# Performance work log

Measured on AMD Instinct MI355X. Metric: run time of the kernel, lower is better.

## Reference

```python
import jax, jax.numpy as jnp
import numpy as np

ALPHA = 0.2  # LeakyReLU negative slope (init arg `alpha`)
N, F_IN, F_OUT = 8192, 512, 256


def setup_inputs() -> dict:
    key = jax.random.key(0)
    k1, k2, k3, k4 = jax.random.split(key, 4)
    x = jax.random.normal(k1, (N, F_IN), dtype=jnp.float32)
    adj = jax.random.randint(k2, (N, N), 0, 2, dtype=jnp.int32)
    W = jax.random.normal(k3, (F_IN, F_OUT), dtype=jnp.float32) * (1.0 / np.sqrt(F_IN))
    a = jax.random.normal(k4, (2 * F_OUT, 1), dtype=jnp.float32) * (1.0 / np.sqrt(F_IN))
    return {"x": x, "adj": adj, "W": W, "a": a}


def reference(x, adj, W, a):
    h = x @ W  # [N, F_OUT]
    f_out = W.shape[1]
    # e[i,j] = LeakyReLU(a1 . h_i + a2 . h_j); computed without the O(N^2*2F) concat
    f1 = h @ a[:f_out, 0]   # [N]
    f2 = h @ a[f_out:, 0]   # [N]
    s = f1[:, None] + f2[None, :]  # [N, N]
    e = jnp.where(s >= 0, s, ALPHA * s)
    # Faithful to the source bug: -9e15 * zeros_like == zeros, so masked entries are 0.0
    att = jnp.where(adj > 0, e, jnp.zeros((), dtype=e.dtype))
    att = jax.nn.softmax(att, axis=1)
    # dropout is identity in eval mode
    h_prime = att @ h  # [N, F_OUT]
    return jax.nn.elu(h_prime)  # concat=True branch
```

## Files before the change

### kernel.cpp

```cpp
#include <hip/hip_runtime.h>
#include <stdint.h>

#define NN 8192
#define FIN 512
#define FOUT 256
#define ALPHA 0.2f
#define KSPLIT 8
#define KSLICE (NN / KSPLIT)
#define BK 32
#define ITERS (KSLICE / BK)

typedef float f32x4 __attribute__((ext_vector_type(4)));
typedef short s16x8 __attribute__((ext_vector_type(8)));

__device__ __forceinline__ uint16_t f2bf(float f) {
  union { float f; uint32_t u; } v; v.f = f;
  uint32_t u = v.u + 0x7fffu + ((v.u >> 16) & 1u);
  return (uint16_t)(u >> 16);
}

__device__ __forceinline__ void lds_barrier() {
  asm volatile("s_waitcnt lgkmcnt(0)\n\ts_barrier" ::: "memory");
}

__global__ __launch_bounds__(256) void k_wa(const float* __restrict__ W,
                                            const float* __restrict__ a,
                                            float* __restrict__ wa1, float* __restrict__ wa2) {
  __shared__ float a1[256], a2[256];
  int tid = threadIdx.x;
  a1[tid] = a[tid];
  a2[tid] = a[tid + 256];
  __syncthreads();
  int m = blockIdx.x * 256 + tid;
  const float* wrow = W + (size_t)m * FOUT;
  float s1 = 0.f, s2 = 0.f;
  for (int k = 0; k < FOUT; k += 4) {
    f32x4 v = *(const f32x4*)(wrow + k);
#pragma unroll
    for (int i = 0; i < 4; i++) {
      s1 += v[i] * a1[k + i];
      s2 += v[i] * a2[k + i];
    }
  }
  wa1[m] = s1; wa2[m] = s2;
}

__global__ __launch_bounds__(256) void k_f1f2(const float* __restrict__ x,
                                              const float* __restrict__ wa1,
                                              const float* __restrict__ wa2,
                                              float* __restrict__ f1, float* __restrict__ f2) {
  __shared__ float s1[512], s2[512];
  int tid = threadIdx.x;
  s1[tid] = wa1[tid]; s1[tid + 256] = wa1[tid + 256];
  s2[tid] = wa2[tid]; s2[tid + 256] = wa2[tid + 256];
  __syncthreads();
  int w = tid >> 6, l = tid & 63;
  int row = blockIdx.x * 4 + w;
  const float* xr = x + (size_t)row * FIN + l * 8;
  f32x4 v0 = *(const f32x4*)xr;
  f32x4 v1 = *(const f32x4*)(xr + 4);
  int kb = l * 8;
  float d1 = 0.f, d2 = 0.f;
#pragma unroll
  for (int i = 0; i < 4; i++) {
    d1 += v0[i] * s1[kb + i] + v1[i] * s1[kb + 4 + i];
    d2 += v0[i] * s2[kb + i] + v1[i] * s2[kb + 4 + i];
  }
#pragma unroll
  for (int off = 32; off; off >>= 1) {
    d1 += __shfl_down(d1, off);
    d2 += __shfl_down(d2, off);
  }
  if (l == 0) { f1[row] = d1; f2[row] = d2; }
}

__global__ __launch_bounds__(256) void k_prep_wt(const float* __restrict__ W,
                                                 uint16_t* __restrict__ wt) {
  int idx = blockIdx.x * 256 + threadIdx.x;
  int f  = idx >> 7;
  int k4 = (idx & 127) * 4;
  ushort4 o;
  o.x = f2bf(W[(size_t)(k4 + 0) * FOUT + f]);
  o.y = f2bf(W[(size_t)(k4 + 1) * FOUT + f]);
  o.z = f2bf(W[(size_t)(k4 + 2) * FOUT + f]);
  o.w = f2bf(W[(size_t)(k4 + 3) * FOUT + f]);
  *(ushort4*)(wt + (size_t)f * FIN + k4) = o;
}

__global__ __launch_bounds__(256, 2) void k_gemm_h(const float* __restrict__ x,
                                                   const uint16_t* __restrict__ wt,
                                                   uint16_t* __restrict__ ht) {
  __shared__ __align__(16) uint16_t Xs[64][40];
  __shared__ __align__(16) uint16_t Ws[128][40];
  int i0 = blockIdx.x * 64;
  int f0 = blockIdx.y * 128;
  int tid = threadIdx.x;
  int l = tid & 63, w = tid >> 6;
  int q = l >> 4, r16 = l & 15;
  f32x4 acc[4][2];
#pragma unroll
  for (int a = 0; a < 4; a++)
#pragma unroll
    for (int b = 0; b < 2; b++) acc[a][b] = (f32x4)0.f;

  int xr = tid >> 2, xc = (tid & 3) * 8;
  int wr = tid >> 1, wc = (tid & 1) * 16;
  const float* xp = x + (size_t)(i0 + xr) * FIN + xc;
  const uint16_t* wp = wt + (size_t)(f0 + wr) * FIN + wc;

  f32x4 u0 = *(const f32x4*)xp;
  f32x4 u1 = *(const f32x4*)(xp + 4);
  uint4 wA = *(const uint4*)wp;
  uint4 wB = *(const uint4*)(wp + 8);

  const int GI = FIN / BK;
  for (int s = 0; s < GI; s++) {
    int sn = (s + 1 < GI) ? (s + 1) : s;
    f32x4 u0n = *(const f32x4*)(xp + sn * BK);
    f32x4 u1n = *(const f32x4*)(xp + sn * BK + 4);
    uint4 wAn = *(const uint4*)(wp + sn * BK);
    uint4 wBn = *(const uint4*)(wp + sn * BK + 8);

    uint4 pk;
    pk.x = (uint32_t)f2bf(u0[0]) | ((uint32_t)f2bf(u0[1]) << 16);
    pk.y = (uint32_t)f2bf(u0[2]) | ((uint32_t)f2bf(u0[3]) << 16);
    pk.z = (uint32_t)f2bf(u1[0]) | ((uint32_t)f2bf(u1[1]) << 16);
    pk.w = (uint32_t)f2bf(u1[2]) | ((uint32_t)f2bf(u1[3]) << 16);
    *(uint4*)(&Xs[xr][xc]) = pk;
    *(uint4*)(&Ws[wr][wc]) = wA;
    *(uint4*)(&Ws[wr][wc + 8]) = wB;
    lds_barrier();

    s16x8 Af[4], Bf[2];
#pragma unroll
    for (int a = 0; a < 4; a++) Af[a] = *(const s16x8*)(&Xs[a * 16 + r16][q * 8]);
#pragma unroll
    for (int b = 0; b < 2; b++) Bf[b] = *(const s16x8*)(&Ws[w * 32 + b * 16 + r16][q * 8]);
#pragma unroll
    for (int a = 0; a < 4; a++)
#pragma unroll
      for (int b = 0; b < 2; b++)
        acc[a][b] = __builtin_amdgcn_mfma_f32_16x16x32_bf16(Af[a], Bf[b], acc[a][b], 0, 0, 0);
    lds_barrier();
    u0 = u0n; u1 = u1n; wA = wAn; wB = wBn;
  }

#pragma unroll
  for (int a = 0; a < 4; a++)
#pragma unroll
    for (int b = 0; b < 2; b++) {
      int f = f0 + w * 32 + b * 16 + r16;
      int i = i0 + a * 16 + q * 4;
      ushort4 o;
      o.x = f2bf(acc[a][b][0]); o.y = f2bf(acc[a][b][1]);
      o.z = f2bf(acc[a][b][2]); o.w = f2bf(acc[a][b][3]);
      *(ushort4*)(ht + (size_t)f * NN + i) = o;
    }
}

__global__ __launch_bounds__(256) void k_zero(float* __restrict__ l_arr) {
  l_arr[blockIdx.x * 256 + threadIdx.x] = 0.f;
}

__global__ __launch_bounds__(256, 3) void k_att(const int* __restrict__ adj,
                                                const uint16_t* __restrict__ ht,
                                                const float* __restrict__ f1,
                                                const float* __restrict__ f2,
                                                float* __restrict__ l_arr,
                                                float* __restrict__ part) {
  __shared__ __align__(16) uint16_t Ps[2][64][40];
  __shared__ __align__(16) float Fs[KSLICE];
  const int i0 = blockIdx.x * 64;
  const int jbase = blockIdx.y * KSLICE;
  const int tid = threadIdx.x;
  const int l = tid & 63, w = tid >> 6;
  const int q = l >> 4, r16 = l & 15;
  const int pr = tid >> 2, pc = tid & 3;

  *(f32x4*)(&Fs[tid * 4]) = *(const f32x4*)(f2 + jbase + tid * 4);

  const float f1i = f1[i0 + pr];
  float lsum = 0.f;
  f32x4 acc[4][4];
#pragma unroll
  for (int a = 0; a < 4; a++)
#pragma unroll
    for (int b = 0; b < 4; b++) acc[a][b] = (f32x4)0.f;

  const int* adjp = adj + (size_t)(i0 + pr) * NN + jbase + pc * 8;
  const uint16_t* htb = ht + (size_t)(w * 64 + r16) * NN + jbase + q * 8;

  int4 adjR0[2], adjR1[2];
  s16x8 Bf0[4], Bf1[4];

#define LOADADJ(t, R) do {                                    \
    int t_ = ((t) < ITERS) ? (t) : (ITERS - 1);               \
    const int* ap_ = adjp + t_ * BK;                          \
    R[0] = *(const int4*)ap_;                                 \
    R[1] = *(const int4*)(ap_ + 4);                           \
  } while (0)

#define LOADB(t, B) do {                                      \
    int t_ = ((t) < ITERS) ? (t) : (ITERS - 1);               \
    const uint16_t* hp_ = htb + t_ * BK;                      \
    B[0] = *(const s16x8*)(hp_);                              \
    B[1] = *(const s16x8*)(hp_ + (size_t)16 * NN);            \
    B[2] = *(const s16x8*)(hp_ + (size_t)32 * NN);            \
    B[3] = *(const s16x8*)(hp_ + (size_t)48 * NN);            \
  } while (0)

#define STAGE(t, R, buf) do {                                 \
    f32x4 F0_ = *(const f32x4*)(&Fs[(t) * BK + pc * 8]);      \
    f32x4 F1_ = *(const f32x4*)(&Fs[(t) * BK + pc * 8 + 4]);  \
    const int* av_ = (const int*)&R[0];                       \
    s16x8 pv_;                                                \
    _Pragma("unroll")                                         \
    for (int i_ = 0; i_ < 8; i_++) {                          \
      float fj_ = (i_ < 4) ? F0_[i_] : F1_[i_ - 4];           \
      float s_ = f1i + fj_;                                   \
      float e_ = fmaxf(s_, ALPHA * s_);                       \
      float p2_ = (av_[i_] != 0) ? __expf(e_) : 1.0f;         \
      lsum += p2_;                                            \
      pv_[i_] = (short)f2bf(p2_);                             \
    }                                                         \
    *(s16x8*)(&Ps[buf][pr][pc * 8]) = pv_;                    \
  } while (0)

#define MFMA_(B, buf) do {                                    \
    s16x8 Af_[4];                                             \
    _Pragma("unroll")                                         \
    for (int a_ = 0; a_ < 4; a_++)                            \
      Af_[a_] = *(const s16x8*)(&Ps[buf][a_ * 16 + r16][q * 8]); \
    _Pragma("unroll")                                         \
    for (int a_ = 0; a_ < 4; a_++)                            \
      _Pragma("unroll")                                       \
      for (int b_ = 0; b_ < 4; b_++)                          \
        acc[a_][b_] = __builtin_amdgcn_mfma_f32_16x16x32_bf16(Af_[a_], B[b_], acc[a_][b_], 0, 0, 0); \
  } while (0)

  LOADADJ(0, adjR0); LOADADJ(1, adjR1);
  LOADB(0, Bf0);     LOADB(1, Bf1);
  lds_barrier();
  STAGE(0, adjR0, 0);
  LOADADJ(2, adjR0);
  lds_barrier();

  for (int s = 0; s < ITERS - 2; s += 2) {
    MFMA_(Bf0, 0);
    LOADB(s + 2, Bf0);
    STAGE(s + 1, adjR1, 1);
    LOADADJ(s + 3, adjR1);
    lds_barrier();

    MFMA_(Bf1, 1);
    LOADB(s + 3, Bf1);
    STAGE(s + 2, adjR0, 0);
    LOADADJ(s + 4, adjR0);
    lds_barrier();
  }
  MFMA_(Bf0, 0);
  STAGE(ITERS - 1, adjR1, 1);
  lds_barrier();
  MFMA_(Bf1, 1);

#undef LOADADJ
#undef LOADB
#undef STAGE
#undef MFMA_

  lsum += __shfl_down(lsum, 2);
  lsum += __shfl_down(lsum, 1);
  if (pc == 0) atomicAdd(&l_arr[i0 + pr], lsum);

  float* pb = part + (size_t)blockIdx.y * ((size_t)NN * FOUT);
#pragma unroll
  for (int a = 0; a < 4; a++)
#pragma unroll
    for (int b = 0; b < 4; b++)
#pragma unroll
      for (int reg = 0; reg < 4; reg++) {
        int row = i0 + a * 16 + q * 4 + reg;
        int col = w * 64 + b * 16 + r16;
        pb[(size_t)row * FOUT + col] = acc[a][b][reg];
      }
}

__global__ __launch_bounds__(256) void k_combine(const float* __restrict__ part,
                                                 const float* __restrict__ l_arr,
                                                 float* __restrict__ out) {
  int idx = (blockIdx.x * 256 + threadIdx.x) * 4;
  float r = 1.0f / l_arr[idx >> 8];
  f32x4 sum = (f32x4)0.f;
#pragma unroll
  for (int p = 0; p < KSPLIT; p++)
    sum += *(const f32x4*)(part + (size_t)p * NN * FOUT + idx);
  f32x4 o;
#pragma unroll
  for (int i = 0; i < 4; i++) {
    float v = sum[i] * r;
    o[i] = v > 0.f ? v : (__expf(v) - 1.f);
  }
  *(f32x4*)(out + idx) = o;
}

extern "C" void kernel_launch(void* const* d_in, const int* in_sizes, int n_in,
                              void* d_out, int out_size, void* d_ws, size_t ws_size,
                              hipStream_t stream) {
  const float* x   = (const float*)d_in[0];
  const int*   adj = (const int*)d_in[1];
  const float* W   = (const float*)d_in[2];
  const float* a   = (const float*)d_in[3];
  float* out = (float*)d_out;

  char* ws = (char*)d_ws;
  float*    wa1   = (float*)ws;
  float*    wa2   = wa1 + 512;
  float*    f1    = wa2 + 512;
  float*    f2    = f1 + NN;
  float*    l_arr = f2 + NN;
  uint16_t* wt    = (uint16_t*)(l_arr + NN);
  uint16_t* ht    = wt + (size_t)FOUT * FIN;
  float*    part  = (float*)(ht + (size_t)NN * FOUT);

  k_wa<<<2, 256, 0, stream>>>(W, a, wa1, wa2);
  k_prep_wt<<<128, 256, 0, stream>>>(W, wt);
  k_f1f2<<<NN / 4, 256, 0, stream>>>(x, wa1, wa2, f1, f2);
  k_zero<<<NN / 256, 256, 0, stream>>>(l_arr);
  k_gemm_h<<<dim3(128, 2), 256, 0, stream>>>(x, wt, ht);
  k_att<<<dim3(NN / 64, KSPLIT), 256, 0, stream>>>(adj, ht, f1, f2, l_arr, part);
  k_combine<<<NN * FOUT / 1024, 256, 0, stream>>>(part, l_arr, out);
}
```

Measured before the change: 470.3 us.

## Pack adjacency to bytes and tile h for contiguous attention-kernel loads

```diff
diff --git a/kernel.cpp b/kernel.cpp
--- a/kernel.cpp
+++ b/kernel.cpp
@@ -87,9 +87,27 @@
   *(ushort4*)(wt + (size_t)f * FIN + k4) = o;
 }
 
+__global__ __launch_bounds__(256) void k_pack(const int* __restrict__ adj,
+                                              uint8_t* __restrict__ adj8) {
+  size_t t = (size_t)blockIdx.x * 256 + threadIdx.x;
+  int i  = (int)(t >> 10);
+  int jc = (int)(t & 1023) * 8;
+  const int4* p = (const int4*)(adj + (size_t)i * NN + jc);
+  int4 v0 = p[0], v1 = p[1];
+  uint64_t bb =  (uint64_t)(v0.x != 0)        | ((uint64_t)(v0.y != 0) << 8)
+              | ((uint64_t)(v0.z != 0) << 16) | ((uint64_t)(v0.w != 0) << 24)
+              | ((uint64_t)(v1.x != 0) << 32) | ((uint64_t)(v1.y != 0) << 40)
+              | ((uint64_t)(v1.z != 0) << 48) | ((uint64_t)(v1.w != 0) << 56);
+  int ib = i >> 6, ri = i & 63;
+  int slice = jc >> 10;
+  int rem = jc & 1023;
+  int s = rem >> 5, c = rem & 31;
+  *(uint64_t*)(adj8 + ((size_t)((ib * KSPLIT + slice) * ITERS + s)) * 2048 + ri * 32 + c) = bb;
+}
+
 __global__ __launch_bounds__(256, 2) void k_gemm_h(const float* __restrict__ x,
                                                    const uint16_t* __restrict__ wt,
-                                                   uint16_t* __restrict__ ht) {
+                                                   uint16_t* __restrict__ htt) {
   __shared__ __align__(16) uint16_t Xs[64][40];
   __shared__ __align__(16) uint16_t Ws[128][40];
   int i0 = blockIdx.x * 64;
@@ -151,10 +169,13 @@
     for (int b = 0; b < 2; b++) {
       int f = f0 + w * 32 + b * 16 + r16;
       int i = i0 + a * 16 + q * 4;
+      int slice = i / KSLICE;
+      int rem = i % KSLICE;
+      int s = rem >> 5, k = rem & 31;
       ushort4 o;
       o.x = f2bf(acc[a][b][0]); o.y = f2bf(acc[a][b][1]);
       o.z = f2bf(acc[a][b][2]); o.w = f2bf(acc[a][b][3]);
-      *(ushort4*)(ht + (size_t)f * NN + i) = o;
+      *(ushort4*)(htt + ((size_t)((slice * ITERS + s) * 256 + f)) * 32 + k) = o;
     }
 }
 
@@ -162,8 +183,8 @@
   l_arr[blockIdx.x * 256 + threadIdx.x] = 0.f;
 }
 
-__global__ __launch_bounds__(256, 3) void k_att(const int* __restrict__ adj,
-                                                const uint16_t* __restrict__ ht,
+__global__ __launch_bounds__(256, 4) void k_att(const uint8_t* __restrict__ adj8,
+                                                const uint16_t* __restrict__ htt,
                                                 const float* __restrict__ f1,
                                                 const float* __restrict__ f2,
                                                 float* __restrict__ l_arr,
@@ -187,39 +208,38 @@
 #pragma unroll
     for (int b = 0; b < 4; b++) acc[a][b] = (f32x4)0.f;
 
-  const int* adjp = adj + (size_t)(i0 + pr) * NN + jbase + pc * 8;
-  const uint16_t* htb = ht + (size_t)(w * 64 + r16) * NN + jbase + q * 8;
-
-  int4 adjR0[2], adjR1[2];
+  const uint8_t* adjp = adj8 +
+      ((size_t)((blockIdx.x * KSPLIT + blockIdx.y) * ITERS)) * 2048 + pr * 32 + pc * 8;
+  const uint16_t* htb = htt + ((size_t)(blockIdx.y * ITERS)) * 8192
+                        + (w * 64 + r16) * 32 + q * 8;
+
+  uint64_t adjR0, adjR1;
   s16x8 Bf0[4], Bf1[4];
 
 #define LOADADJ(t, R) do {                                    \
     int t_ = ((t) < ITERS) ? (t) : (ITERS - 1);               \
-    const int* ap_ = adjp + t_ * BK;                          \
-    R[0] = *(const int4*)ap_;                                 \
-    R[1] = *(const int4*)(ap_ + 4);                           \
+    R = *(const uint64_t*)(adjp + (size_t)t_ * 2048);         \
   } while (0)
 
 #define LOADB(t, B) do {                                      \
     int t_ = ((t) < ITERS) ? (t) : (ITERS - 1);               \
-    const uint16_t* hp_ = htb + t_ * BK;                      \
+    const uint16_t* hp_ = htb + (size_t)t_ * 8192;            \
     B[0] = *(const s16x8*)(hp_);                              \
-    B[1] = *(const s16x8*)(hp_ + (size_t)16 * NN);            \
-    B[2] = *(const s16x8*)(hp_ + (size_t)32 * NN);            \
-    B[3] = *(const s16x8*)(hp_ + (size_t)48 * NN);            \
+    B[1] = *(const s16x8*)(hp_ + 512);                        \
+    B[2] = *(const s16x8*)(hp_ + 1024);                       \
+    B[3] = *(const s16x8*)(hp_ + 1536);                       \
   } while (0)
 
 #define STAGE(t, R, buf) do {                                 \
     f32x4 F0_ = *(const f32x4*)(&Fs[(t) * BK + pc * 8]);      \
     f32x4 F1_ = *(const f32x4*)(&Fs[(t) * BK + pc * 8 + 4]);  \
-    const int* av_ = (const int*)&R[0];                       \
     s16x8 pv_;                                                \
     _Pragma("unroll")                                         \
     for (int i_ = 0; i_ < 8; i_++) {                          \
       float fj_ = (i_ < 4) ? F0_[i_] : F1_[i_ - 4];           \
       float s_ = f1i + fj_;                                   \
       float e_ = fmaxf(s_, ALPHA * s_);                       \
-      float p2_ = (av_[i_] != 0) ? __expf(e_) : 1.0f;         \
+      float p2_ = (((R) >> (8 * i_)) & 0xffull) ? __expf(e_) : 1.0f; \
       lsum += p2_;                                            \
       pv_[i_] = (short)f2bf(p2_);                             \
     }                                                         \
@@ -319,14 +339,16 @@
   float*    f2    = f1 + NN;
   float*    l_arr = f2 + NN;
   uint16_t* wt    = (uint16_t*)(l_arr + NN);
-  uint16_t* ht    = wt + (size_t)FOUT * FIN;
-  float*    part  = (float*)(ht + (size_t)NN * FOUT);
+  uint16_t* htt   = wt + (size_t)FOUT * FIN;
+  uint8_t*  adj8  = (uint8_t*)(htt + (size_t)NN * FOUT);
+  float*    part  = (float*)(adj8 + (size_t)NN * NN / 8 * 8);
 
   k_wa<<<2, 256, 0, stream>>>(W, a, wa1, wa2);
   k_prep_wt<<<128, 256, 0, stream>>>(W, wt);
   k_f1f2<<<NN / 4, 256, 0, stream>>>(x, wa1, wa2, f1, f2);
   k_zero<<<NN / 256, 256, 0, stream>>>(l_arr);
-  k_gemm_h<<<dim3(128, 2), 256, 0, stream>>>(x, wt, ht);
-  k_att<<<dim3(NN / 64, KSPLIT), 256, 0, stream>>>(adj, ht, f1, f2, l_arr, part);
+  k_pack<<<(int)((size_t)NN * NN / 8 / 256), 256, 0, stream>>>(adj, adj8);
+  k_gemm_h<<<dim3(128, 2), 256, 0, stream>>>(x, wt, htt);
+  k_att<<<dim3(NN / 64, KSPLIT), 256, 0, stream>>>(adj8, htt, f1, f2, l_arr, part);
   k_combine<<<NN * FOUT / 1024, 256, 0, stream>>>(part, l_arr, out);
 }
```

Measured after the change: 498.9 us. +6.1%, slower.
